# Optimization experiments

Hardware: AMD Instinct MI355X
Metric: run time of the kernel (lower is better)

## Reference

```python
import jax, jax.numpy as jnp
import numpy as np

EPS = 1e-3  # Q = eps * I(5) in the original module

def setup_inputs() -> dict:
    key = jax.random.key(0)
    k1, k2, k3 = jax.random.split(key, 3)
    B, n = 4194304, 5
    x = jax.random.normal(k1, (B, n), dtype=jnp.float32)
    # fc1 = nn.Linear(n, n): weight [n, n], bias [n]
    W = jax.random.normal(k2, (n, n), dtype=jnp.float32) * (1.0 / np.sqrt(n))
    b_fc = jax.random.normal(k3, (n,), dtype=jnp.float32) * 0.1
    return {"x": x, "W": W, "b_fc": b_fc}

def reference(x, W, b_fc):
    # h = fc1(x)  (the QP inequality RHS per sample)
    h = x @ W.T + b_fc  # [B, 5]
    # Per-sample QP: min_z 0.5*eps*||z||^2 + 1^T z  s.t.  -z <= h  (G = -I)
    # Separable closed form (exact solution cvxopt converges to):
    #   unconstrained minimizer z_i = -1/eps; constraint z_i >= -h_i
    #   => z_i = max(-h_i, -1/eps)
    z = jnp.maximum(-h, -1.0 / EPS)  # [B, 5] primal solutions
    return z
```

## Files before the change

kernel.cpp:

```cpp
#include <hip/hip_runtime.h>


#define ROWS_PER_THREAD 4
#define BLOCK 256

__global__ __launch_bounds__(BLOCK) void qpnet_kernel(
    const float* __restrict__ x,
    const float* __restrict__ W,
    const float* __restrict__ bfc,
    float* __restrict__ out,
    int n_groups)
{
    float w[5][5];
    float bias[5];
#pragma unroll
    for (int j = 0; j < 5; ++j) {
        bias[j] = bfc[j];
#pragma unroll
        for (int i = 0; i < 5; ++i) {
            w[j][i] = W[j * 5 + i];
        }
    }

    const int stride = gridDim.x * BLOCK;
    for (int t = blockIdx.x * BLOCK + threadIdx.x; t < n_groups; t += stride) {
        const float4* __restrict__ xin  = reinterpret_cast<const float4*>(x) + (size_t)t * 5;
        float4* __restrict__       zout = reinterpret_cast<float4*>(out)     + (size_t)t * 5;

        float v[20];
        *reinterpret_cast<float4*>(&v[0])  = xin[0];
        *reinterpret_cast<float4*>(&v[4])  = xin[1];
        *reinterpret_cast<float4*>(&v[8])  = xin[2];
        *reinterpret_cast<float4*>(&v[12]) = xin[3];
        *reinterpret_cast<float4*>(&v[16]) = xin[4];

        float o[20];
#pragma unroll
        for (int k = 0; k < 4; ++k) {
#pragma unroll
            for (int j = 0; j < 5; ++j) {
                float h = bias[j];
#pragma unroll
                for (int i = 0; i < 5; ++i) {
                    h = fmaf(v[k * 5 + i], w[j][i], h);
                }
                o[k * 5 + j] = fmaxf(-h, -1000.0f);
            }
        }

        zout[0] = *reinterpret_cast<float4*>(&o[0]);
        zout[1] = *reinterpret_cast<float4*>(&o[4]);
        zout[2] = *reinterpret_cast<float4*>(&o[8]);
        zout[3] = *reinterpret_cast<float4*>(&o[12]);
        zout[4] = *reinterpret_cast<float4*>(&o[16]);
    }
}

extern "C" void kernel_launch(void* const* d_in, const int* in_sizes, int n_in,
                              void* d_out, int out_size, void* d_ws, size_t ws_size,
                              hipStream_t stream) {
    const float* x   = (const float*)d_in[0];
    const float* W   = (const float*)d_in[1];
    const float* bfc = (const float*)d_in[2];
    float* out = (float*)d_out;

    int B = in_sizes[0] / 5;
    int n_groups = B / ROWS_PER_THREAD;
    int grid = (n_groups + BLOCK - 1) / BLOCK;

    qpnet_kernel<<<grid, BLOCK, 0, stream>>>(x, W, bfc, out, n_groups);
}
```

Measured before the change: 159.9 us.

## Stage input and output through LDS for fully coalesced float4 global access

Each block now loads a contiguous tile of float4 values with consecutive threads reading consecutive addresses, scatters them into LDS with a rotated layout to reduce bank conflicts, computes the 5x5 affine plus clamp per row from LDS, and writes results back through LDS with coalesced stores. This replaces the per-thread 80-byte strided accesses of the old layout. It adds two block barriers and 20KB of LDS per block, which may limit occupancy.

```diff
diff --git a/kernel.cpp b/kernel.cpp
--- a/kernel.cpp
+++ b/kernel.cpp
@@ -1,58 +1,101 @@
 #include <hip/hip_runtime.h>
 
 
-#define ROWS_PER_THREAD 4
 #define BLOCK 256
+#define F4_PER_THREAD 5
+#define TILE_F4 (BLOCK * F4_PER_THREAD)
+#define LDS_WORDS (BLOCK * 20)
+
+__device__ __forceinline__ int lds_addr(int g, int p) {
+    int r = g % 5;
+    int s = p + r;
+    if (s >= 5) s -= 5;
+    return g * 20 + 4 * s;
+}
 
 __global__ __launch_bounds__(BLOCK) void qpnet_kernel(
     const float* __restrict__ x,
     const float* __restrict__ W,
     const float* __restrict__ bfc,
     float* __restrict__ out,
-    int n_groups)
+    int total_f4)
 {
+    __shared__ __align__(16) float lds[LDS_WORDS];
+
     float w[5][5];
     float bias[5];
 #pragma unroll
     for (int j = 0; j < 5; ++j) {
         bias[j] = bfc[j];
 #pragma unroll
-        for (int i = 0; i < 5; ++i) {
-            w[j][i] = W[j * 5 + i];
+        for (int i = 0; i < 5; ++i) w[j][i] = W[j * 5 + i];
+    }
+
+    const int tid = threadIdx.x;
+    const int tile_base = blockIdx.x * TILE_F4;
+    const float4* __restrict__ xin  = reinterpret_cast<const float4*>(x);
+    float4* __restrict__       zout = reinterpret_cast<float4*>(out);
+
+#pragma unroll
+    for (int k = 0; k < F4_PER_THREAD; ++k) {
+        int f = k * BLOCK + tid;
+        int gf = tile_base + f;
+        if (gf < total_f4) {
+            float4 val = xin[gf];
+            int g = f / 5, p = f - g * 5;
+            *reinterpret_cast<float4*>(&lds[lds_addr(g, p)]) = val;
         }
     }
+    __syncthreads();
 
-    const int stride = gridDim.x * BLOCK;
-    for (int t = blockIdx.x * BLOCK + threadIdx.x; t < n_groups; t += stride) {
-        const float4* __restrict__ xin  = reinterpret_cast<const float4*>(x) + (size_t)t * 5;
-        float4* __restrict__       zout = reinterpret_cast<float4*>(out)     + (size_t)t * 5;
+    float v[20];
+    {
+        int r = tid % 5;
+#pragma unroll
+        for (int p = 0; p < 5; ++p) {
+            int s = p + r; if (s >= 5) s -= 5;
+            *reinterpret_cast<float4*>(&v[4 * p]) =
+                *reinterpret_cast<const float4*>(&lds[tid * 20 + 4 * s]);
+        }
+    }
+#pragma unroll
+    for (int k = 0; k < 4; ++k) {
+        float t0, t1, t2, t3, t4;
+        t0 = bias[0]; t1 = bias[1]; t2 = bias[2]; t3 = bias[3]; t4 = bias[4];
+#pragma unroll
+        for (int i = 0; i < 5; ++i) {
+            float xv = v[k * 5 + i];
+            t0 = fmaf(xv, w[0][i], t0);
+            t1 = fmaf(xv, w[1][i], t1);
+            t2 = fmaf(xv, w[2][i], t2);
+            t3 = fmaf(xv, w[3][i], t3);
+            t4 = fmaf(xv, w[4][i], t4);
+        }
+        v[k * 5 + 0] = fmaxf(-t0, -1000.0f);
+        v[k * 5 + 1] = fmaxf(-t1, -1000.0f);
+        v[k * 5 + 2] = fmaxf(-t2, -1000.0f);
+        v[k * 5 + 3] = fmaxf(-t3, -1000.0f);
+        v[k * 5 + 4] = fmaxf(-t4, -1000.0f);
+    }
+    {
+        int r = tid % 5;
+#pragma unroll
+        for (int p = 0; p < 5; ++p) {
+            int s = p + r; if (s >= 5) s -= 5;
+            *reinterpret_cast<float4*>(&lds[tid * 20 + 4 * s]) =
+                *reinterpret_cast<const float4*>(&v[4 * p]);
+        }
+    }
+    __syncthreads();
 
-        float v[20];
-        *reinterpret_cast<float4*>(&v[0])  = xin[0];
-        *reinterpret_cast<float4*>(&v[4])  = xin[1];
-        *reinterpret_cast<float4*>(&v[8])  = xin[2];
-        *reinterpret_cast<float4*>(&v[12]) = xin[3];
-        *reinterpret_cast<float4*>(&v[16]) = xin[4];
-
-        float o[20];
 #pragma unroll
-        for (int k = 0; k < 4; ++k) {
-#pragma unroll
-            for (int j = 0; j < 5; ++j) {
-                float h = bias[j];
-#pragma unroll
-                for (int i = 0; i < 5; ++i) {
-                    h = fmaf(v[k * 5 + i], w[j][i], h);
-                }
-                o[k * 5 + j] = fmaxf(-h, -1000.0f);
-            }
+    for (int k = 0; k < F4_PER_THREAD; ++k) {
+        int f = k * BLOCK + tid;
+        int gf = tile_base + f;
+        if (gf < total_f4) {
+            int g = f / 5, p = f - g * 5;
+            zout[gf] = *reinterpret_cast<const float4*>(&lds[lds_addr(g, p)]);
         }
-
-        zout[0] = *reinterpret_cast<float4*>(&o[0]);
-        zout[1] = *reinterpret_cast<float4*>(&o[4]);
-        zout[2] = *reinterpret_cast<float4*>(&o[8]);
-        zout[3] = *reinterpret_cast<float4*>(&o[12]);
-        zout[4] = *reinterpret_cast<float4*>(&o[16]);
     }
 }
 
@@ -64,9 +107,8 @@
     const float* bfc = (const float*)d_in[2];
     float* out = (float*)d_out;
 
-    int B = in_sizes[0] / 5;
-    int n_groups = B / ROWS_PER_THREAD;
-    int grid = (n_groups + BLOCK - 1) / BLOCK;
+    int total_f4 = in_sizes[0] / 4;
+    int grid = (total_f4 + TILE_F4 - 1) / TILE_F4;
 
-    qpnet_kernel<<<grid, BLOCK, 0, stream>>>(x, W, bfc, out, n_groups);
+    qpnet_kernel<<<grid, BLOCK, 0, stream>>>(x, W, bfc, out, total_f4);
 }
```

New measurement: 153.8 us. 1.04x faster.

## Map threads to aligned 16-float output chunks with halo-loaded input windows

Applied to the files above, without the earlier changes.

Each thread now produces four contiguous float4 outputs (16 floats) and reads a six-float4 window that covers the rows overlapping those outputs, dispatching on t%5 to a templated compute variant. Output stores become nontemporal. The aim is to make consecutive lanes touch consecutive 64-byte segments for better coalescing and to stop output writes from polluting the cache. The cost is 20% redundant input loads, divergence across the five switch cases within a wave, and roughly 80 FMAs per thread for 16 outputs.

```diff
diff --git a/kernel.cpp b/kernel.cpp
--- a/kernel.cpp
+++ b/kernel.cpp
@@ -1,15 +1,34 @@
 #include <hip/hip_runtime.h>
 
 
-#define ROWS_PER_THREAD 4
 #define BLOCK 256
+
+typedef float vf4 __attribute__((ext_vector_type(4)));
+
+template <int S>
+__device__ __forceinline__ void compute_case(const float* __restrict__ win,
+                                             const float (&w)[5][5],
+                                             const float (&bias)[5],
+                                             float* __restrict__ o) {
+#pragma unroll
+    for (int m = 0; m < 16; ++m) {
+        const int r  = (S + m) / 5;
+        const int c  = (S + m) % 5;
+        const int wb = 4 - S + 5 * r;
+        float h = bias[c];
+#pragma unroll
+        for (int i = 0; i < 5; ++i) h = fmaf(win[wb + i], w[c][i], h);
+        o[m] = fmaxf(-h, -1000.0f);
+    }
+}
 
 __global__ __launch_bounds__(BLOCK) void qpnet_kernel(
     const float* __restrict__ x,
     const float* __restrict__ W,
     const float* __restrict__ bfc,
     float* __restrict__ out,
-    int n_groups)
+    int n_threads,
+    int total_f4)
 {
     float w[5][5];
     float bias[5];
@@ -17,43 +36,43 @@
     for (int j = 0; j < 5; ++j) {
         bias[j] = bfc[j];
 #pragma unroll
-        for (int i = 0; i < 5; ++i) {
-            w[j][i] = W[j * 5 + i];
-        }
+        for (int i = 0; i < 5; ++i) w[j][i] = W[j * 5 + i];
     }
 
-    const int stride = gridDim.x * BLOCK;
-    for (int t = blockIdx.x * BLOCK + threadIdx.x; t < n_groups; t += stride) {
-        const float4* __restrict__ xin  = reinterpret_cast<const float4*>(x) + (size_t)t * 5;
-        float4* __restrict__       zout = reinterpret_cast<float4*>(out)     + (size_t)t * 5;
+    const int t = blockIdx.x * BLOCK + threadIdx.x;
+    if (t >= n_threads) return;
 
-        float v[20];
-        *reinterpret_cast<float4*>(&v[0])  = xin[0];
-        *reinterpret_cast<float4*>(&v[4])  = xin[1];
-        *reinterpret_cast<float4*>(&v[8])  = xin[2];
-        *reinterpret_cast<float4*>(&v[12]) = xin[3];
-        *reinterpret_cast<float4*>(&v[16]) = xin[4];
+    const vf4* __restrict__ xin  = reinterpret_cast<const vf4*>(x);
+    vf4* __restrict__       zout = reinterpret_cast<vf4*>(out);
 
-        float o[20];
-#pragma unroll
-        for (int k = 0; k < 4; ++k) {
-#pragma unroll
-            for (int j = 0; j < 5; ++j) {
-                float h = bias[j];
-#pragma unroll
-                for (int i = 0; i < 5; ++i) {
-                    h = fmaf(v[k * 5 + i], w[j][i], h);
-                }
-                o[k * 5 + j] = fmaxf(-h, -1000.0f);
-            }
-        }
+    float win[24];
+    const int lo = 4 * t - 1;
+    {
+        int i0 = lo < 0 ? 0 : lo;
+        int i5 = lo + 5;
+        if (i5 > total_f4 - 1) i5 = total_f4 - 1;
+        *reinterpret_cast<vf4*>(&win[0])  = xin[i0];
+        *reinterpret_cast<vf4*>(&win[4])  = xin[lo + 1];
+        *reinterpret_cast<vf4*>(&win[8])  = xin[lo + 2];
+        *reinterpret_cast<vf4*>(&win[12]) = xin[lo + 3];
+        *reinterpret_cast<vf4*>(&win[16]) = xin[lo + 4];
+        *reinterpret_cast<vf4*>(&win[20]) = xin[i5];
+    }
 
-        zout[0] = *reinterpret_cast<float4*>(&o[0]);
-        zout[1] = *reinterpret_cast<float4*>(&o[4]);
-        zout[2] = *reinterpret_cast<float4*>(&o[8]);
-        zout[3] = *reinterpret_cast<float4*>(&o[12]);
-        zout[4] = *reinterpret_cast<float4*>(&o[16]);
+    float o[16];
+    switch (t % 5) {
+        case 0: compute_case<0>(win, w, bias, o); break;
+        case 1: compute_case<1>(win, w, bias, o); break;
+        case 2: compute_case<2>(win, w, bias, o); break;
+        case 3: compute_case<3>(win, w, bias, o); break;
+        default: compute_case<4>(win, w, bias, o); break;
     }
+
+    const int ob = 4 * t;
+    __builtin_nontemporal_store(*reinterpret_cast<vf4*>(&o[0]),  &zout[ob + 0]);
+    __builtin_nontemporal_store(*reinterpret_cast<vf4*>(&o[4]),  &zout[ob + 1]);
+    __builtin_nontemporal_store(*reinterpret_cast<vf4*>(&o[8]),  &zout[ob + 2]);
+    __builtin_nontemporal_store(*reinterpret_cast<vf4*>(&o[12]), &zout[ob + 3]);
 }
 
 extern "C" void kernel_launch(void* const* d_in, const int* in_sizes, int n_in,
@@ -64,9 +83,9 @@
     const float* bfc = (const float*)d_in[2];
     float* out = (float*)d_out;
 
-    int B = in_sizes[0] / 5;
-    int n_groups = B / ROWS_PER_THREAD;
-    int grid = (n_groups + BLOCK - 1) / BLOCK;
+    int total_f4  = in_sizes[0] / 4;
+    int n_threads = total_f4 / 4;
+    int grid = (n_threads + BLOCK - 1) / BLOCK;
 
-    qpnet_kernel<<<grid, BLOCK, 0, stream>>>(x, W, bfc, out, n_groups);
+    qpnet_kernel<<<grid, BLOCK, 0, stream>>>(x, W, bfc, out, n_threads, total_f4);
 }
```

After: 173.7 us. 8.7% more time.
